# Kernel optimization log

Hardware: AMD Instinct MI355X
Metric: run time of the kernel (lower is better)

Reference implementation:

```python
import jax, jax.numpy as jnp
from jax import lax
import numpy as np

ARG_NAMES = ('x w1 b1 bn1_g bn1_b bn1_m bn1_v w2 b2 bn2_g bn2_b bn2_m bn2_v w3 b3 w4 b4 '
             'attn_w attn_b attn_u g0_w1 g0_b1 g0_w2 g0_b2 g1_w1 g1_b1 g1_w2 g1_b2 '
             'g2_w1 g2_b1 g2_w2 g2_b2 c_w1 c_b1 c_w2 c_b2 c_w3 c_b3 c_w4 c_b4').split()


def _conv1d(x, w, b, stride, pad):
    # x: [N, C, L], w: [O, I, K]
    y = lax.conv_general_dilated(x, w, (stride,), [(pad, pad)],
                                 dimension_numbers=('NCH', 'OIH', 'NCH'))
    return y + b[None, :, None]


def _bn(x, g, b, m, v, eps=1e-5):
    # eval-mode BatchNorm1d over channel dim of [N, C, L]
    inv = g / jnp.sqrt(v + eps)
    return (x - m[None, :, None]) * inv[None, :, None] + b[None, :, None]


def _forward(x, w1, b1, bn1_g, bn1_b, bn1_m, bn1_v, w2, b2, bn2_g, bn2_b, bn2_m, bn2_v,
             w3, b3, w4, b4, attn_w, attn_b, attn_u,
             g0_w1, g0_b1, g0_w2, g0_b2, g1_w1, g1_b1, g1_w2, g1_b2,
             g2_w1, g2_b1, g2_w2, g2_b2,
             c_w1, c_b1, c_w2, c_b2, c_w3, c_b3, c_w4, c_b4):
    B, S, C, T = x.shape  # [batch, crops, channels=64, time=400]
    h = x.reshape(-1, C, T)
    # CNN stack (dropout = identity in eval)
    h = _bn(jax.nn.elu(_conv1d(h, w1, b1, 2, 1)), bn1_g, bn1_b, bn1_m, bn1_v)   # [N,64,192]
    h = _bn(jax.nn.elu(_conv1d(h, w2, b2, 2, 0)), bn2_g, bn2_b, bn2_m, bn2_v)   # [N,64,87]
    h = jax.nn.elu(_conv1d(h, w3, b3, 1, 0))                                    # [N,64,82]
    h = lax.reduce_window(h, 0.0, lax.add, (1, 1, 3), (1, 1, 2), 'VALID') / 3.0  # [N,64,40]
    h = jax.nn.elu(_conv1d(h, w4, b4, 1, 0))                                    # [N,64,35]
    h = h.reshape(B, S, C, -1)  # [B, S, 64, 35]
    # Attention pooling over the crop dim (dim=1), sum=True
    v = jnp.tanh(jnp.einsum('bsch,hd->bscd', h, attn_w) + attn_b)
    alphas = jax.nn.softmax(jnp.einsum('bscd,d->bsc', v, attn_u), axis=1)
    h = jax.nn.elu((h * alphas[..., None]).sum(axis=1))  # [B, 64, 35]
    # GIN over complete 64-node graph (self-loops included, eps=0):
    # aggregation per node == sum over all nodes of the graph
    def gin(h, W1, B1, W2, B2):
        agg = h + h.sum(axis=1, keepdims=True)
        return jax.nn.relu(agg @ W1 + B1) @ W2 + B2
    h = jax.nn.relu(gin(h, g0_w1, g0_b1, g0_w2, g0_b2))
    h = jax.nn.relu(gin(h, g1_w1, g1_b1, g1_w2, g1_b2))
    h = gin(h, g2_w1, g2_b1, g2_w2, g2_b2)  # no act after last layer
    # Classifier
    f = h.reshape(B, -1)  # [B, 2240]
    f = jax.nn.elu(f @ c_w1 + c_b1)
    f = jax.nn.elu(f @ c_w2 + c_b2)
    f = jax.nn.elu(f @ c_w3 + c_b3)
    return f @ c_w4 + c_b4  # [B, 2]


def setup_inputs() -> dict:
    key = jax.random.key(0)
    ks = iter(jax.random.split(key, 64))
    def rn(shape, s=0.05):
        return jax.random.normal(next(ks), shape, dtype=jnp.float32) * s
    d = {}
    d['x'] = jax.random.normal(next(ks), (32, 16, 64, 400), dtype=jnp.float32)
    d['w1'] = rn((64, 64, 20)); d['b1'] = rn((64,))
    d['bn1_g'] = jnp.ones((64,), jnp.float32); d['bn1_b'] = jnp.zeros((64,), jnp.float32)
    d['bn1_m'] = jnp.zeros((64,), jnp.float32); d['bn1_v'] = jnp.ones((64,), jnp.float32)
    d['w2'] = rn((64, 64, 20)); d['b2'] = rn((64,))
    d['bn2_g'] = jnp.ones((64,), jnp.float32); d['bn2_b'] = jnp.zeros((64,), jnp.float32)
    d['bn2_m'] = jnp.zeros((64,), jnp.float32); d['bn2_v'] = jnp.ones((64,), jnp.float32)
    d['w3'] = rn((64, 64, 6)); d['b3'] = rn((64,))
    d['w4'] = rn((64, 64, 6)); d['b4'] = rn((64,))
    d['attn_w'] = rn((35, 256), 0.1); d['attn_b'] = rn((256,), 0.1); d['attn_u'] = rn((256,), 0.1)
    d['g0_w1'] = rn((35, 256)); d['g0_b1'] = rn((256,))
    d['g0_w2'] = rn((256, 256)); d['g0_b2'] = rn((256,))
    d['g1_w1'] = rn((256, 256)); d['g1_b1'] = rn((256,))
    d['g1_w2'] = rn((256, 256)); d['g1_b2'] = rn((256,))
    d['g2_w1'] = rn((256, 35)); d['g2_b1'] = rn((35,))
    d['g2_w2'] = rn((35, 35)); d['g2_b2'] = rn((35,))
    d['c_w1'] = rn((2240, 256)); d['c_b1'] = rn((256,))
    d['c_w2'] = rn((256, 64)); d['c_b2'] = rn((64,))
    d['c_w3'] = rn((64, 16)); d['c_b3'] = rn((16,))
    d['c_w4'] = rn((16, 2)); d['c_b4'] = rn((2,))
    return d


def reference(x, w1, b1, bn1_g, bn1_b, bn1_m, bn1_v, w2, b2, bn2_g, bn2_b, bn2_m, bn2_v,
              w3, b3, w4, b4, attn_w, attn_b, attn_u,
              g0_w1, g0_b1, g0_w2, g0_b2, g1_w1, g1_b1, g1_w2, g1_b2,
              g2_w1, g2_b1, g2_w2, g2_b2,
              c_w1, c_b1, c_w2, c_b2, c_w3, c_b3, c_w4, c_b4):
    return _forward(x, w1, b1, bn1_g, bn1_b, bn1_m, bn1_v, w2, b2, bn2_g, bn2_b, bn2_m, bn2_v,
                    w3, b3, w4, b4, attn_w, attn_b, attn_u,
                    g0_w1, g0_b1, g0_w2, g0_b2, g1_w1, g1_b1, g1_w2, g1_b2,
                    g2_w1, g2_b1, g2_w2, g2_b2,
                    c_w1, c_b1, c_w2, c_b2, c_w3, c_b3, c_w4, c_b4)
```

## Files before the change

kernel.cpp:

```cpp
#include <hip/hip_runtime.h>
#include <math.h>

typedef __attribute__((ext_vector_type(8))) __bf16 bf16x8;
typedef __attribute__((ext_vector_type(4))) __bf16 bf16x4;
typedef __attribute__((ext_vector_type(4))) float f32x4;

__device__ __forceinline__ float elu_f(float v) {
    return v > 0.f ? v : (expf(v) - 1.f);
}

__global__ __launch_bounds__(256) void prep_weights(
    const float* __restrict__ w1, const float* __restrict__ w2,
    const float* __restrict__ w3, const float* __restrict__ w4,
    __bf16* __restrict__ t1, __bf16* __restrict__ t2,
    __bf16* __restrict__ t3, __bf16* __restrict__ t4)
{
    int idx = blockIdx.x * 256 + threadIdx.x;
    if (idx < 81920) {
        int k = idx / 4096, r = idx - k * 4096, co = r >> 6, ci = r & 63;
        t1[idx] = (__bf16)w1[(co * 64 + ci) * 20 + k];
    } else if (idx < 163840) {
        int j = idx - 81920;
        int k = j / 4096, r = j - k * 4096, co = r >> 6, ci = r & 63;
        t2[j] = (__bf16)w2[(co * 64 + ci) * 20 + k];
    } else if (idx < 188416) {
        int j = idx - 163840;
        int k = j / 4096, r = j - k * 4096, co = r >> 6, ci = r & 63;
        t3[j] = (__bf16)w3[(co * 64 + ci) * 6 + k];
    } else if (idx < 212992) {
        int j = idx - 188416;
        int k = j / 4096, r = j - k * 4096, co = r >> 6, ci = r & 63;
        t4[j] = (__bf16)w4[(co * 64 + ci) * 6 + k];
    }
}

__global__ __launch_bounds__(256) void prep_tr(
    const float* __restrict__ g0w1, const float* __restrict__ g0w2,
    const float* __restrict__ g1w1, const float* __restrict__ g1w2,
    const float* __restrict__ g2w1, const float* __restrict__ g2w2,
    __bf16* __restrict__ d0, __bf16* __restrict__ d1, __bf16* __restrict__ d2,
    __bf16* __restrict__ d3, __bf16* __restrict__ d4, __bf16* __restrict__ d5)
{
    int bid = blockIdx.x;
    const float* src; __bf16* dst; int K, O, Kpad, Opad, tile;
    if (bid < 4)       { src = g0w1; dst = d0; K = 35;   O = 256; Kpad = 64;   Opad = 256; tile = bid; }
    else if (bid < 20) { src = g0w2; dst = d1; K = 256;  O = 256; Kpad = 256;  Opad = 256; tile = bid - 4; }
    else if (bid < 36) { src = g1w1; dst = d2; K = 256;  O = 256; Kpad = 256;  Opad = 256; tile = bid - 20; }
    else if (bid < 52) { src = g1w2; dst = d3; K = 256;  O = 256; Kpad = 256;  Opad = 256; tile = bid - 36; }
    else if (bid < 56) { src = g2w1; dst = d4; K = 256;  O = 35;  Kpad = 256;  Opad = 64;  tile = bid - 52; }
    else               { src = g2w2; dst = d5; K = 35;   O = 35;  Kpad = 64;   Opad = 64;  tile = 0; }
    int ktiles = Kpad >> 6;
    int ot = tile / ktiles, kt = tile - ot * ktiles;
    int k0 = kt * 64, o0 = ot * 64;
    size_t LOFF = (size_t)Opad * Kpad;
    __shared__ float tl[64][68];
    int c = threadIdx.x & 63, rr = threadIdx.x >> 6;
    #pragma unroll
    for (int it = 0; it < 16; ++it) {
        int r = rr + it * 4;
        int kk = k0 + r, oo = o0 + c;
        tl[r][c] = (kk < K && oo < O) ? src[(size_t)kk * O + oo] : 0.f;
    }
    __syncthreads();
    #pragma unroll
    for (int it = 0; it < 16; ++it) {
        int r = rr + it * 4;
        float v = tl[c][r];
        __bf16 hi = (__bf16)v;
        float lo = v - (float)hi;
        size_t pos = (size_t)(o0 + r) * Kpad + k0 + c;
        dst[pos] = hi;
        dst[LOFF + pos] = (__bf16)lo;
    }
}

__global__ __launch_bounds__(256, 2) void conv1_mfma(
    const float* __restrict__ x, const __bf16* __restrict__ wT,
    const float* __restrict__ bias,
    const float* __restrict__ bn_g, const float* __restrict__ bn_b,
    const float* __restrict__ bn_m, const float* __restrict__ bn_v,
    __bf16* __restrict__ y)
{
    constexpr int LIN = 400, LOUT = 192, PAD = 1;
    constexpr int ROWS = 201;
    __shared__ __align__(16) __bf16 sx[2 * ROWS * 72];

    const int tid = threadIdx.x;
    const int n = blockIdx.x;
    const int wave = tid >> 6, lane = tid & 63;
    const int m = lane & 15, quad = lane >> 4;

    {
        const float* xg = x + (size_t)n * 64 * LIN;
        if (tid < 128) {
            int v = (tid >> 6) ? 401 : 0;
            sx[((v & 1) * ROWS + (v >> 1)) * 72 + (tid & 63)] = (__bf16)0.f;
        }
        constexpr int ITEMS = 16 * (LIN / 4);
        #pragma unroll
        for (int it = 0; it < 7; ++it) {
            int idx = it * 256 + tid;
            if (idx < ITEMS) {
                int jj = idx & 3;
                int g  = (idx >> 2) & 15;
                int q  = (idx >> 6) * 4 + jj;
                const float* xp = xg + (size_t)(4 * g) * LIN + 4 * q;
                float fa[4][4];
                #pragma unroll
                for (int u = 0; u < 4; ++u)
                    *(float4*)&fa[u][0] = *(const float4*)(xp + (size_t)u * LIN);
                #pragma unroll
                for (int e = 0; e < 4; ++e) {
                    int v = 4 * q + e + PAD;
                    bf16x4 wv = { (__bf16)fa[0][e], (__bf16)fa[1][e],
                                  (__bf16)fa[2][e], (__bf16)fa[3][e] };
                    *(bf16x4*)&sx[((v & 1) * ROWS + (v >> 1)) * 72 + 4 * g] = wv;
                }
            }
        }
    }

    const __bf16* wb = wT + (size_t)(wave * 16 + m) * 64 + quad * 8;
    bf16x8 bw[20][2];
    #pragma unroll
    for (int kp = 0; kp < 20; ++kp)
        #pragma unroll
        for (int s = 0; s < 2; ++s)
            bw[kp][s] = *(const bf16x8*)(wb + (size_t)kp * 4096 + s * 32);

    __syncthreads();

    const int co = wave * 16 + m;
    const float bi = bias[co];
    const float inv   = bn_g[co] / sqrtf(bn_v[co] + 1e-5f);
    const float shift = bn_b[co] - bn_m[co] * inv;

    for (int mo = 0; mo < 4; ++mo) {
        f32x4 acc[3];
        #pragma unroll
        for (int mi = 0; mi < 3; ++mi) acc[mi] = (f32x4){0.f, 0.f, 0.f, 0.f};

        #pragma unroll
        for (int kp = 0; kp < 20; ++kp) {
            const int buf = kp & 1, rowoff = kp >> 1;
            const __bf16* abase = sx + ((size_t)buf * ROWS + mo * 48 + m + rowoff) * 72;
            #pragma unroll
            for (int s = 0; s < 2; ++s) {
                bf16x8 af[3];
                #pragma unroll
                for (int mi = 0; mi < 3; ++mi)
                    af[mi] = *(const bf16x8*)(abase + mi * (16 * 72) + s * 32 + quad * 8);
                #pragma unroll
                for (int mi = 0; mi < 3; ++mi)
                    acc[mi] = __builtin_amdgcn_mfma_f32_16x16x32_bf16(
                        af[mi], bw[kp][s], acc[mi], 0, 0, 0);
            }
        }

        #pragma unroll
        for (int mi = 0; mi < 3; ++mi)
            #pragma unroll
            for (int r = 0; r < 4; ++r) {
                int t = mo * 48 + mi * 16 + quad * 4 + r;
                float v = elu_f(acc[mi][r] + bi) * inv + shift;
                y[((size_t)n * LOUT + t) * 64 + co] = (__bf16)v;
            }
    }
}

__global__ __launch_bounds__(512, 2) void conv234_fused(
    const __bf16* __restrict__ h1,
    const __bf16* __restrict__ wT2, const float* __restrict__ b2,
    const float* __restrict__ bn2g, const float* __restrict__ bn2b,
    const float* __restrict__ bn2m, const float* __restrict__ bn2v,
    const __bf16* __restrict__ wT3, const float* __restrict__ b3,
    const __bf16* __restrict__ wT4, const float* __restrict__ b4,
    __bf16* __restrict__ h4)
{
    __shared__ __align__(16) __bf16 bufA[2 * 96 * 72];
    __shared__ __align__(16) __bf16 bufB[87 * 72];

    const int tid = threadIdx.x;
    const int n = blockIdx.x;
    const int wave = tid >> 6, lane = tid & 63;
    const int m = lane & 15, quad = lane >> 4;
    const int th  = wave >> 2;
    const int coq = wave & 3;

    {
        const __bf16* src = h1 + (size_t)n * 192 * 64;
        #pragma unroll
        for (int it = 0; it < 3; ++it) {
            int idx = it * 512 + tid;
            int v = idx >> 3, c8 = (idx & 7) * 8;
            *(uint4*)(bufA + ((size_t)(v & 1) * 96 + (v >> 1)) * 72 + c8) =
                *(const uint4*)(src + (size_t)v * 64 + c8);
        }
    }
    __syncthreads();

    {
        const __bf16* wb = wT2 + (size_t)(coq * 16 + m) * 64 + quad * 8;
        bf16x8 bw[20][2];
        #pragma unroll
        for (int kp = 0; kp < 20; ++kp)
            #pragma unroll
            for (int s = 0; s < 2; ++s)
                bw[kp][s] = *(const bf16x8*)(wb + (size_t)kp * 4096 + s * 32);

        f32x4 acc[3];
        #pragma unroll
        for (int mi = 0; mi < 3; ++mi) acc[mi] = (f32x4){0.f, 0.f, 0.f, 0.f};

        #pragma unroll
        for (int kp = 0; kp < 20; ++kp) {
            const int buf = kp & 1, rowoff = kp >> 1;
            const int r0 = th * 48 + m + rowoff;
            #pragma unroll
            for (int s = 0; s < 2; ++s) {
                bf16x8 af[3];
                #pragma unroll
                for (int mi = 0; mi < 3; ++mi) {
                    int rr = r0 + mi * 16; if (rr > 95) rr = 95;
                    af[mi] = *(const bf16x8*)(bufA + ((size_t)buf * 96 + rr) * 72 + s * 32 + quad * 8);
                }
                #pragma unroll
                for (int mi = 0; mi < 3; ++mi)
                    acc[mi] = __builtin_amdgcn_mfma_f32_16x16x32_bf16(
                        af[mi], bw[kp][s], acc[mi], 0, 0, 0);
            }
        }

        const int co = coq * 16 + m;
        const float bi = b2[co];
        float inv = bn2g[co] / sqrtf(bn2v[co] + 1e-5f);
        float shift = bn2b[co] - bn2m[co] * inv;
        #pragma unroll
        for (int mi = 0; mi < 3; ++mi)
            #pragma unroll
            for (int r = 0; r < 4; ++r) {
                int t = th * 48 + mi * 16 + quad * 4 + r;
                if (t < 87) {
                    float v = elu_f(acc[mi][r] + bi) * inv + shift;
                    bufB[t * 72 + co] = (__bf16)v;
                }
            }
    }
    __syncthreads();

    {
        const __bf16* wb = wT3 + (size_t)(coq * 16 + m) * 64 + quad * 8;
        bf16x8 bw[6][2];
        #pragma unroll
        for (int kp = 0; kp < 6; ++kp)
            #pragma unroll
            for (int s = 0; s < 2; ++s)
                bw[kp][s] = *(const bf16x8*)(wb + (size_t)kp * 4096 + s * 32);

        f32x4 acc[3];
        #pragma unroll
        for (int mi = 0; mi < 3; ++mi) acc[mi] = (f32x4){0.f, 0.f, 0.f, 0.f};

        #pragma unroll
        for (int kp = 0; kp < 6; ++kp) {
            const int r0 = th * 48 + m + kp;
            #pragma unroll
            for (int s = 0; s < 2; ++s) {
                bf16x8 af[3];
                #pragma unroll
                for (int mi = 0; mi < 3; ++mi) {
                    int rr = r0 + mi * 16; if (rr > 86) rr = 86;
                    af[mi] = *(const bf16x8*)(bufB + (size_t)rr * 72 + s * 32 + quad * 8);
                }
                #pragma unroll
                for (int mi = 0; mi < 3; ++mi)
                    acc[mi] = __builtin_amdgcn_mfma_f32_16x16x32_bf16(
                        af[mi], bw[kp][s], acc[mi], 0, 0, 0);
            }
        }

        const int co = coq * 16 + m;
        const float bi = b3[co];
        #pragma unroll
        for (int mi = 0; mi < 3; ++mi)
            #pragma unroll
            for (int r = 0; r < 4; ++r) {
                int t = th * 48 + mi * 16 + quad * 4 + r;
                if (t < 82)
                    bufA[t * 72 + co] = (__bf16)elu_f(acc[mi][r] + bi);
            }
    }
    __syncthreads();

    #pragma unroll
    for (int it = 0; it < 5; ++it) {
        int idx = it * 512 + tid;
        int t = idx >> 6, co = idx & 63;
        float v = ((float)bufA[(2 * t) * 72 + co] + (float)bufA[(2 * t + 1) * 72 + co] +
                   (float)bufA[(2 * t + 2) * 72 + co]) * (1.f / 3.f);
        bufB[t * 72 + co] = (__bf16)v;
    }
    __syncthreads();

    if (wave < 4) {
        const int co0 = wave * 16;
        const __bf16* wb = wT4 + (size_t)(co0 + m) * 64 + quad * 8;
        bf16x8 bw[6][2];
        #pragma unroll
        for (int kp = 0; kp < 6; ++kp)
            #pragma unroll
            for (int s = 0; s < 2; ++s)
                bw[kp][s] = *(const bf16x8*)(wb + (size_t)kp * 4096 + s * 32);

        f32x4 acc4[3];
        #pragma unroll
        for (int mi = 0; mi < 3; ++mi) acc4[mi] = (f32x4){0.f, 0.f, 0.f, 0.f};

        #pragma unroll
        for (int kp = 0; kp < 6; ++kp) {
            const int r0 = m + kp;
            #pragma unroll
            for (int s = 0; s < 2; ++s) {
                bf16x8 af[3];
                #pragma unroll
                for (int mi = 0; mi < 3; ++mi) {
                    int rr = r0 + mi * 16; if (rr > 39) rr = 39;
                    af[mi] = *(const bf16x8*)(bufB + (size_t)rr * 72 + s * 32 + quad * 8);
                }
                #pragma unroll
                for (int mi = 0; mi < 3; ++mi)
                    acc4[mi] = __builtin_amdgcn_mfma_f32_16x16x32_bf16(
                        af[mi], bw[kp][s], acc4[mi], 0, 0, 0);
            }
        }

        const int co = co0 + m;
        const float bi = b4[co];
        #pragma unroll
        for (int mi = 0; mi < 3; ++mi)
            #pragma unroll
            for (int r = 0; r < 4; ++r) {
                int t = mi * 16 + quad * 4 + r;
                if (t < 35)
                    h4[((size_t)n * 35 + t) * 64 + co] = (__bf16)elu_f(acc4[mi][r] + bi);
            }
    }
}

__global__ __launch_bounds__(256) void attn_pool_k(
    const __bf16* __restrict__ h, const float* __restrict__ W,
    const float* __restrict__ ab, const float* __restrict__ u,
    float* __restrict__ out)
{
    __shared__ float sW[35 * 256];
    __shared__ float sh[4][16 * 35 + 5];
    const int tid = threadIdx.x;
    const int pair0 = blockIdx.x * 4;
    for (int i = tid; i < 35 * 256; i += 256) sW[i] = W[i];
    for (int i = tid; i < 4 * 560; i += 256) {
        int q = i / 560, r = i - q * 560;
        int s = r / 35, t = r - s * 35;
        int bc = pair0 + q, b = bc >> 6, c = bc & 63;
        sh[q][s * 35 + t] = (float)h[(((size_t)b * 16 + s) * 35 + t) * 64 + c];
    }
    __syncthreads();

    const int wave = tid >> 6, lane = tid & 63;
    const int bc = pair0 + wave;
    const float* shw = sh[wave];

    float myu[4], myb[4];
    #pragma unroll
    for (int p = 0; p < 4; ++p) { myu[p] = u[lane + 64 * p]; myb[p] = ab[lane + 64 * p]; }

    float dot[16][4];
    #pragma unroll
    for (int s = 0; s < 16; ++s)
        #pragma unroll
        for (int p = 0; p < 4; ++p) dot[s][p] = myb[p];

    for (int t = 0; t < 35; ++t) {
        float w0 = sW[t * 256 + lane];
        float w1 = sW[t * 256 + lane + 64];
        float w2 = sW[t * 256 + lane + 128];
        float w3 = sW[t * 256 + lane + 192];
        #pragma unroll
        for (int s = 0; s < 16; ++s) {
            float hv = shw[s * 35 + t];
            dot[s][0] = fmaf(hv, w0, dot[s][0]);
            dot[s][1] = fmaf(hv, w1, dot[s][1]);
            dot[s][2] = fmaf(hv, w2, dot[s][2]);
            dot[s][3] = fmaf(hv, w3, dot[s][3]);
        }
    }

    float sc[16];
    #pragma unroll
    for (int s = 0; s < 16; ++s) {
        float v = tanhf(dot[s][0]) * myu[0] + tanhf(dot[s][1]) * myu[1]
                + tanhf(dot[s][2]) * myu[2] + tanhf(dot[s][3]) * myu[3];
        #pragma unroll
        for (int off = 1; off < 64; off <<= 1) v += __shfl_xor(v, off, 64);
        sc[s] = v;
    }

    float mx = sc[0];
    #pragma unroll
    for (int s = 1; s < 16; ++s) mx = fmaxf(mx, sc[s]);
    float e[16], sum = 0.f;
    #pragma unroll
    for (int s = 0; s < 16; ++s) { e[s] = expf(sc[s] - mx); sum += e[s]; }
    float inv = 1.f / sum;

    if (lane < 35) {
        float acc = 0.f;
        #pragma unroll
        for (int s = 0; s < 16; ++s) acc = fmaf(shw[s * 35 + lane], e[s] * inv, acc);
        out[(size_t)bc * 35 + lane] = elu_f(acc);
    }
}

#define APLANE (64 * 264)

__device__ __forceinline__ void gin_gemm_dev(
    const __bf16* As,
    const __bf16* __restrict__ Wg, int Kpad, int wlo, int Kout,
    const float* __restrict__ bias,
    int mode, __bf16* Ad, float* __restrict__ outg)
{
    const int lane = threadIdx.x & 63;
    const int wave = threadIdx.x >> 6;
    const int o0 = wave * 32;
    if (o0 >= ((Kout + 63) & ~63)) return;
    const int m = lane & 15, quad = lane >> 4;

    f32x4 acc[4][2];
    #pragma unroll
    for (int mi = 0; mi < 4; ++mi)
        #pragma unroll
        for (int nj = 0; nj < 2; ++nj)
            acc[mi][nj] = (f32x4){0.f, 0.f, 0.f, 0.f};

    for (int k0 = 0; k0 < Kpad; k0 += 32) {
        bf16x8 ah[4], al[4], bh[2], bl[2];
        #pragma unroll
        for (int mi = 0; mi < 4; ++mi) {
            const __bf16* ap = As + (size_t)(mi * 16 + m) * 264 + k0 + quad * 8;
            ah[mi] = *(const bf16x8*)ap;
            al[mi] = *(const bf16x8*)(ap + APLANE);
        }
        #pragma unroll
        for (int nj = 0; nj < 2; ++nj) {
            const __bf16* wp = Wg + (size_t)(o0 + nj * 16 + m) * Kpad + k0 + quad * 8;
            bh[nj] = *(const bf16x8*)wp;
            bl[nj] = *(const bf16x8*)(wp + wlo);
        }
        #pragma unroll
        for (int mi = 0; mi < 4; ++mi)
            #pragma unroll
            for (int nj = 0; nj < 2; ++nj) {
                acc[mi][nj] = __builtin_amdgcn_mfma_f32_16x16x32_bf16(
                    al[mi], bh[nj], acc[mi][nj], 0, 0, 0);
                acc[mi][nj] = __builtin_amdgcn_mfma_f32_16x16x32_bf16(
                    ah[mi], bl[nj], acc[mi][nj], 0, 0, 0);
                acc[mi][nj] = __builtin_amdgcn_mfma_f32_16x16x32_bf16(
                    ah[mi], bh[nj], acc[mi][nj], 0, 0, 0);
            }
    }

    #pragma unroll
    for (int nj = 0; nj < 2; ++nj) {
        const int o = o0 + nj * 16 + m;
        const bool ovalid = (o < Kout);
        const float bi = ovalid ? bias[o] : 0.f;
        float v[4][4];
        #pragma unroll
        for (int mi = 0; mi < 4; ++mi)
            #pragma unroll
            for (int r = 0; r < 4; ++r)
                v[mi][r] = acc[mi][nj][r] + bi;
        if (mode == 2) {
            if (ovalid) {
                #pragma unroll
                for (int mi = 0; mi < 4; ++mi)
                    #pragma unroll
                    for (int r = 0; r < 4; ++r)
                        outg[(size_t)(mi * 16 + quad * 4 + r) * Kout + o] = v[mi][r];
            }
        } else {
            float s = 0.f;
            #pragma unroll
            for (int mi = 0; mi < 4; ++mi)
                #pragma unroll
                for (int r = 0; r < 4; ++r) {
                    float rv = ovalid ? fmaxf(v[mi][r], 0.f) : 0.f;
                    v[mi][r] = rv;
                    s += rv;
                }
            if (mode == 1) {
                s += __shfl_xor(s, 16, 64);
                s += __shfl_xor(s, 32, 64);
            } else {
                s = 0.f;
            }
            #pragma unroll
            for (int mi = 0; mi < 4; ++mi)
                #pragma unroll
                for (int r = 0; r < 4; ++r) {
                    float a = v[mi][r] + s;
                    __bf16 hi = (__bf16)a;
                    size_t pos = (size_t)(mi * 16 + quad * 4 + r) * 264 + o;
                    Ad[pos] = hi;
                    Ad[APLANE + pos] = (__bf16)(a - (float)hi);
                }
        }
    }
}

__global__ __launch_bounds__(512) void gin_fused(
    const float* __restrict__ ha,
    const __bf16* __restrict__ gW0a, const __bf16* __restrict__ gW0b,
    const __bf16* __restrict__ gW1a, const __bf16* __restrict__ gW1b,
    const __bf16* __restrict__ gW2a, const __bf16* __restrict__ gW2b,
    const float* __restrict__ b0a, const float* __restrict__ b0b,
    const float* __restrict__ b1a, const float* __restrict__ b1b,
    const float* __restrict__ b2a, const float* __restrict__ b2b,
    float* __restrict__ H3)
{
    const int b = blockIdx.x, tid = threadIdx.x;
    __shared__ __align__(16) __bf16 sA[2][2 * APLANE];
    __shared__ float sS[64];
    const float* hab = ha + (size_t)b * 2240;

    if (tid < 64) {
        float s = 0.f;
        if (tid < 35)
            for (int n = 0; n < 64; ++n) s += hab[n * 35 + tid];
        sS[tid] = s;
    }
    __syncthreads();
    for (int idx = tid; idx < 64 * 64; idx += 512) {
        int n = idx >> 6, k = idx & 63;
        float a = (k < 35) ? hab[n * 35 + k] + sS[k] : 0.f;
        __bf16 hi = (__bf16)a;
        sA[0][n * 264 + k] = hi;
        sA[0][APLANE + n * 264 + k] = (__bf16)(a - (float)hi);
    }
    __syncthreads();

    gin_gemm_dev(sA[0], gW0a, 64,  16384, 256, b0a, 0, sA[1], nullptr); __syncthreads();
    gin_gemm_dev(sA[1], gW0b, 256, 65536, 256, b0b, 1, sA[0], nullptr); __syncthreads();
    gin_gemm_dev(sA[0], gW1a, 256, 65536, 256, b1a, 0, sA[1], nullptr); __syncthreads();
    gin_gemm_dev(sA[1], gW1b, 256, 65536, 256, b1b, 1, sA[0], nullptr); __syncthreads();
    gin_gemm_dev(sA[0], gW2a, 256, 16384, 35,  b2a, 0, sA[1], nullptr); __syncthreads();
    gin_gemm_dev(sA[1], gW2b, 64,  4096,  35,  b2b, 2, nullptr, H3 + (size_t)b * 2240);
}

__global__ __launch_bounds__(256) void cls1_part_k(
    const float* __restrict__ H3, const float* __restrict__ w1,
    float* __restrict__ s1p)
{
    const int b  = blockIdx.x;
    const int kc = blockIdx.y;
    const int k0 = kc * 140;
    __shared__ float sH[140];
    const int tid = threadIdx.x;
    if (tid < 140) sH[tid] = H3[(size_t)b * 2240 + k0 + tid];
    __syncthreads();
    const int o = (tid >> 6) * 64 + (tid & 63);
    float a0 = 0.f, a1 = 0.f, a2 = 0.f, a3 = 0.f;
    const float* wr = w1 + (size_t)k0 * 256 + o;
    #pragma unroll
    for (int k = 0; k < 140; k += 4) {
        a0 = fmaf(sH[k],     wr[(size_t)k * 256],       a0);
        a1 = fmaf(sH[k + 1], wr[(size_t)(k + 1) * 256], a1);
        a2 = fmaf(sH[k + 2], wr[(size_t)(k + 2) * 256], a2);
        a3 = fmaf(sH[k + 3], wr[(size_t)(k + 3) * 256], a3);
    }
    s1p[((size_t)kc * 32 + b) * 256 + o] = a0 + a1 + a2 + a3;
}

__global__ __launch_bounds__(256) void cls234_k(
    const float* __restrict__ s1p, const float* __restrict__ b1,
    const float* __restrict__ w2, const float* __restrict__ b2,
    const float* __restrict__ w3, const float* __restrict__ b3,
    const float* __restrict__ w4, const float* __restrict__ b4,
    float* __restrict__ out)
{
    const int b = blockIdx.x, tid = threadIdx.x;
    __shared__ float s1[256];
    __shared__ float part[4][64];
    __shared__ float s2[64];
    __shared__ float s3[16];
    {
        float acc = b1[tid];
        #pragma unroll
        for (int kc = 0; kc < 16; ++kc)
            acc += s1p[((size_t)kc * 32 + b) * 256 + tid];
        s1[tid] = elu_f(acc);
    }
    __syncthreads();
    {
        int kg = tid >> 6, o = tid & 63;
        float acc = 0.f;
        for (int k = kg * 64; k < kg * 64 + 64; ++k)
            acc = fmaf(s1[k], w2[k * 64 + o], acc);
        part[kg][o] = acc;
    }
    __syncthreads();
    if (tid < 64) {
        float acc = part[0][tid] + part[1][tid] + part[2][tid] + part[3][tid] + b2[tid];
        s2[tid] = elu_f(acc);
    }
    __syncthreads();
    if (tid < 16) {
        float acc = b3[tid];
        for (int k = 0; k < 64; ++k) acc = fmaf(s2[k], w3[k * 16 + tid], acc);
        s3[tid] = elu_f(acc);
    }
    __syncthreads();
    if (tid < 2) {
        float acc = b4[tid];
        for (int k = 0; k < 16; ++k) acc = fmaf(s3[k], w4[k * 2 + tid], acc);
        out[b * 2 + tid] = acc;
    }
}

extern "C" void kernel_launch(void* const* d_in, const int* in_sizes, int n_in,
                              void* d_out, int out_size, void* d_ws, size_t ws_size,
                              hipStream_t stream)
{
    const float* x     = (const float*)d_in[0];
    const float* w1    = (const float*)d_in[1];
    const float* b1    = (const float*)d_in[2];
    const float* bn1_g = (const float*)d_in[3];
    const float* bn1_b = (const float*)d_in[4];
    const float* bn1_m = (const float*)d_in[5];
    const float* bn1_v = (const float*)d_in[6];
    const float* w2    = (const float*)d_in[7];
    const float* b2    = (const float*)d_in[8];
    const float* bn2_g = (const float*)d_in[9];
    const float* bn2_b = (const float*)d_in[10];
    const float* bn2_m = (const float*)d_in[11];
    const float* bn2_v = (const float*)d_in[12];
    const float* w3    = (const float*)d_in[13];
    const float* b3    = (const float*)d_in[14];
    const float* w4    = (const float*)d_in[15];
    const float* b4    = (const float*)d_in[16];
    const float* attn_w = (const float*)d_in[17];
    const float* attn_b = (const float*)d_in[18];
    const float* attn_u = (const float*)d_in[19];
    const float* g0_w1 = (const float*)d_in[20];
    const float* g0_b1 = (const float*)d_in[21];
    const float* g0_w2 = (const float*)d_in[22];
    const float* g0_b2 = (const float*)d_in[23];
    const float* g1_w1 = (const float*)d_in[24];
    const float* g1_b1 = (const float*)d_in[25];
    const float* g1_w2 = (const float*)d_in[26];
    const float* g1_b2 = (const float*)d_in[27];
    const float* g2_w1 = (const float*)d_in[28];
    const float* g2_b1 = (const float*)d_in[29];
    const float* g2_w2 = (const float*)d_in[30];
    const float* g2_b2 = (const float*)d_in[31];
    const float* c_w1  = (const float*)d_in[32];
    const float* c_b1  = (const float*)d_in[33];
    const float* c_w2  = (const float*)d_in[34];
    const float* c_b2  = (const float*)d_in[35];
    const float* c_w3  = (const float*)d_in[36];
    const float* c_b3  = (const float*)d_in[37];
    const float* c_w4  = (const float*)d_in[38];
    const float* c_b4  = (const float*)d_in[39];
    float* out = (float*)d_out;

    char* ws = (char*)d_ws;
    __bf16* wT1  = (__bf16*)(ws + 0);
    __bf16* wT2  = (__bf16*)(ws + 163840);
    __bf16* wT3  = (__bf16*)(ws + 327680);
    __bf16* wT4  = (__bf16*)(ws + 376832);
    __bf16* h1   = (__bf16*)(ws + 425984);
    __bf16* h4   = (__bf16*)(ws + 13008896);
    float*  ha   = (float*)(ws + 15302656);
    __bf16* gW0a = (__bf16*)(ws + 15589376);
    __bf16* gW0b = (__bf16*)(ws + 15654912);
    __bf16* gW1a = (__bf16*)(ws + 15917056);
    __bf16* gW1b = (__bf16*)(ws + 16179200);
    __bf16* gW2a = (__bf16*)(ws + 16441344);
    __bf16* gW2b = (__bf16*)(ws + 16506880);
    float*  H3   = (float*)(ws + 16523264);
    float*  s1p  = (float*)(ws + 16809984);

    prep_weights<<<dim3(832), dim3(256), 0, stream>>>(w1, w2, w3, w4, wT1, wT2, wT3, wT4);
    prep_tr<<<dim3(57), dim3(256), 0, stream>>>(g0_w1, g0_w2, g1_w1, g1_w2, g2_w1, g2_w2,
                                                gW0a, gW0b, gW1a, gW1b, gW2a, gW2b);

    conv1_mfma<<<dim3(512), dim3(256), 0, stream>>>(
        x, wT1, b1, bn1_g, bn1_b, bn1_m, bn1_v, h1);

    conv234_fused<<<dim3(512), dim3(512), 0, stream>>>(
        h1, wT2, b2, bn2_g, bn2_b, bn2_m, bn2_v, wT3, b3, wT4, b4, h4);

    attn_pool_k<<<dim3(512), dim3(256), 0, stream>>>(h4, attn_w, attn_b, attn_u, ha);

    gin_fused<<<dim3(32), dim3(512), 0, stream>>>(
        ha, gW0a, gW0b, gW1a, gW1b, gW2a, gW2b,
        g0_b1, g0_b2, g1_b1, g1_b2, g2_b1, g2_b2, H3);

    cls1_part_k<<<dim3(32, 16), dim3(256), 0, stream>>>(H3, c_w1, s1p);
    cls234_k<<<dim3(32), dim3(256), 0, stream>>>(s1p, c_b1, c_w2, c_b2, c_w3, c_b3,
                                                 c_w4, c_b4, out);
}
```

Before: 300.8 us.

## Repartition conv1 MFMA work so each wave owns a time tile over all channels

In the first conv kernel, work is now split across waves by time tile: each wave handles a 48-timestep tile for all 64 output channels, where before each wave handled 16 channels over all four time tiles. Each A fragment read from LDS now feeds four MFMAs instead of one, which cuts LDS read traffic. Weight fragments are no longer held in registers for all 20 taps; they are streamed from global memory with a two-deep register double buffer. The trade-off is more global/L2 weight loads and 12 accumulator tiles per wave, which raises register pressure.

```diff
diff --git a/kernel.cpp b/kernel.cpp
--- a/kernel.cpp
+++ b/kernel.cpp
@@ -120,49 +120,66 @@
         }
     }
 
-    const __bf16* wb = wT + (size_t)(wave * 16 + m) * 64 + quad * 8;
-    bf16x8 bw[20][2];
-    #pragma unroll
-    for (int kp = 0; kp < 20; ++kp)
+    const __bf16* wb = wT + (size_t)m * 64 + quad * 8;
+    bf16x8 bb[2][2][4];
+    #pragma unroll
+    for (int p = 0; p < 2; ++p)
         #pragma unroll
         for (int s = 0; s < 2; ++s)
-            bw[kp][s] = *(const bf16x8*)(wb + (size_t)kp * 4096 + s * 32);
-
-    __syncthreads();
-
-    const int co = wave * 16 + m;
-    const float bi = bias[co];
-    const float inv   = bn_g[co] / sqrtf(bn_v[co] + 1e-5f);
-    const float shift = bn_b[co] - bn_m[co] * inv;
-
-    for (int mo = 0; mo < 4; ++mo) {
-        f32x4 acc[3];
-        #pragma unroll
-        for (int mi = 0; mi < 3; ++mi) acc[mi] = (f32x4){0.f, 0.f, 0.f, 0.f};
-
-        #pragma unroll
-        for (int kp = 0; kp < 20; ++kp) {
-            const int buf = kp & 1, rowoff = kp >> 1;
-            const __bf16* abase = sx + ((size_t)buf * ROWS + mo * 48 + m + rowoff) * 72;
-            #pragma unroll
-            for (int s = 0; s < 2; ++s) {
-                bf16x8 af[3];
-                #pragma unroll
-                for (int mi = 0; mi < 3; ++mi)
-                    af[mi] = *(const bf16x8*)(abase + mi * (16 * 72) + s * 32 + quad * 8);
-                #pragma unroll
-                for (int mi = 0; mi < 3; ++mi)
-                    acc[mi] = __builtin_amdgcn_mfma_f32_16x16x32_bf16(
-                        af[mi], bw[kp][s], acc[mi], 0, 0, 0);
-            }
-        }
-
+            #pragma unroll
+            for (int nj = 0; nj < 4; ++nj)
+                bb[p][s][nj] = *(const bf16x8*)(wb + (size_t)p * 4096 +
+                                                nj * (16 * 64) + s * 32);
+
+    __syncthreads();
+
+    const int tile = wave;
+    f32x4 acc[3][4];
+    #pragma unroll
+    for (int mi = 0; mi < 3; ++mi)
+        #pragma unroll
+        for (int nj = 0; nj < 4; ++nj)
+            acc[mi][nj] = (f32x4){0.f, 0.f, 0.f, 0.f};
+
+    #pragma unroll
+    for (int kp = 0; kp < 20; ++kp) {
+        const int buf = kp & 1, rowoff = kp >> 1;
+        const __bf16* abase = sx + ((size_t)buf * ROWS + tile * 48 + m + rowoff) * 72;
+        #pragma unroll
+        for (int s = 0; s < 2; ++s) {
+            bf16x8 af[3];
+            #pragma unroll
+            for (int mi = 0; mi < 3; ++mi)
+                af[mi] = *(const bf16x8*)(abase + mi * (16 * 72) + s * 32 + quad * 8);
+            #pragma unroll
+            for (int mi = 0; mi < 3; ++mi)
+                #pragma unroll
+                for (int nj = 0; nj < 4; ++nj)
+                    acc[mi][nj] = __builtin_amdgcn_mfma_f32_16x16x32_bf16(
+                        af[mi], bb[kp & 1][s][nj], acc[mi][nj], 0, 0, 0);
+        }
+        if (kp + 2 < 20) {
+            #pragma unroll
+            for (int s = 0; s < 2; ++s)
+                #pragma unroll
+                for (int nj = 0; nj < 4; ++nj)
+                    bb[kp & 1][s][nj] = *(const bf16x8*)(wb + (size_t)(kp + 2) * 4096 +
+                                                         nj * (16 * 64) + s * 32);
+        }
+    }
+
+    #pragma unroll
+    for (int nj = 0; nj < 4; ++nj) {
+        const int co = nj * 16 + m;
+        const float bi = bias[co];
+        const float inv   = bn_g[co] / sqrtf(bn_v[co] + 1e-5f);
+        const float shift = bn_b[co] - bn_m[co] * inv;
         #pragma unroll
         for (int mi = 0; mi < 3; ++mi)
             #pragma unroll
             for (int r = 0; r < 4; ++r) {
-                int t = mo * 48 + mi * 16 + quad * 4 + r;
-                float v = elu_f(acc[mi][r] + bi) * inv + shift;
+                int t = tile * 48 + mi * 16 + quad * 4 + r;
+                float v = elu_f(acc[mi][nj][r] + bi) * inv + shift;
                 y[((size_t)n * LOUT + t) * 64 + co] = (__bf16)v;
             }
     }
```

After: 317.4 us. +5.5%, slower.
